# Performance work log

Measured on AMD Instinct MI355X. Metric: run time of the kernel, lower is better.

Reference implementation:

```python
import jax, jax.numpy as jnp
import numpy as np

NUM_CLASSES = 21
OVERLAP_THRESH = 0.5
POS_PRIOR_THRESH = 0.01
NEGPOS_RATIO = 3
ARM_VAR = (0.1, 0.2)
VAR = (0.1, 0.2)
B, P, NOBJ = 64, 16320, 32


def _iou(a, b):
    # a: [N,4] point-form, b: [P,4] point-form -> [N,P]
    lt = jnp.maximum(a[:, None, :2], b[None, :, :2])
    rb = jnp.minimum(a[:, None, 2:], b[None, :, 2:])
    wh = jnp.clip(rb - lt, 0.0)
    inter = wh[..., 0] * wh[..., 1]
    area_a = (a[:, 2] - a[:, 0]) * (a[:, 3] - a[:, 1])
    area_b = (b[:, 2] - b[:, 0]) * (b[:, 3] - b[:, 1])
    return inter / (area_a[:, None] + area_b[None, :] - inter)


def _decode_point(loc, priors, var):
    # loc: [P,4], priors: [P,4] center-form -> [P,4] point-form
    cxcy = priors[:, :2] + loc[:, :2] * var[0] * priors[:, 2:]
    wh = priors[:, 2:] * jnp.exp(loc[:, 2:] * var[1])
    return jnp.concatenate([cxcy - wh / 2, cxcy + wh / 2], axis=-1)


def _encode(matched, priors, var):
    # matched: [P,4] point-form gt, priors: [P,4] center-form -> [P,4]
    g_cxcy = ((matched[:, :2] + matched[:, 2:]) / 2 - priors[:, :2]) / (var[0] * priors[:, 2:])
    g_wh = jnp.log((matched[:, 2:] - matched[:, :2]) / priors[:, 2:]) / var[1]
    return jnp.concatenate([g_cxcy, g_wh], axis=-1)


def _match_one(truths, labels, dec_point, ref_center, reserve):
    # truths:[N,4] labels:[N] dec_point/ref_center:[P,4] reserve:[P] bool
    n_obj = truths.shape[0]
    ov = _iou(truths, dec_point)                       # [N,P]
    ovm = jnp.where(reserve[None, :], ov, -1.0)        # mask out filtered priors
    best_prior_idx = jnp.argmax(ovm, axis=1)           # [N]
    best_truth_overlap = jnp.max(ovm, axis=0)          # [P]
    best_truth_idx = jnp.argmax(ovm, axis=0)           # [P]
    best_truth_overlap = best_truth_overlap.at[best_prior_idx].set(2.0)
    best_truth_idx = best_truth_idx.at[best_prior_idx].set(jnp.arange(n_obj))
    matched = truths[best_truth_idx]                   # [P,4]
    conf = labels[best_truth_idx] + 1                  # [P]
    conf = jnp.where(best_truth_overlap < OVERLAP_THRESH, 0, conf)
    loc = _encode(matched, ref_center, VAR)
    conf = jnp.where(reserve, conf, -1)                # ignored priors
    loc = jnp.where(reserve[:, None], loc, 0.0)
    return loc, conf


def setup_inputs() -> dict:
    key = jax.random.key(0)
    ks = jax.random.split(key, 8)
    arm_loc = 0.1 * jax.random.normal(ks[0], (B, P, 4), dtype=jnp.float32)
    arm_conf = jax.random.normal(ks[1], (B, P, 2), dtype=jnp.float32)
    odm_loc = jax.random.normal(ks[2], (B, P, 4), dtype=jnp.float32)
    odm_conf = jax.random.normal(ks[3], (B, P, NUM_CLASSES), dtype=jnp.float32)
    # center-form anchors: valid cx,cy,w,h
    cxcy = jax.random.uniform(ks[4], (P, 2), minval=0.02, maxval=0.98)
    wh = jax.random.uniform(ks[5], (P, 2), minval=0.05, maxval=0.4)
    priors = jnp.concatenate([cxcy, wh], axis=-1).astype(jnp.float32)
    # valid point-form ground-truth boxes
    tc = jax.random.uniform(ks[6], (B, NOBJ, 2), minval=0.2, maxval=0.8)
    tw = jax.random.uniform(ks[7], (B, NOBJ, 2), minval=0.05, maxval=0.3)
    truths = jnp.concatenate([tc - tw / 2, tc + tw / 2], axis=-1).astype(jnp.float32)
    labels = jax.random.randint(jax.random.fold_in(key, 9), (B, NOBJ), 0, 20)
    return {"arm_loc": arm_loc, "arm_conf": arm_conf, "odm_loc": odm_loc,
            "odm_conf": odm_conf, "priors": priors, "truths": truths,
            "labels": labels}


def reference(arm_loc, arm_conf, odm_loc, odm_conf, priors, truths, labels):
    # ARM branch and targets are constants w.r.t. gradients (torch uses .data)
    arm_loc = jax.lax.stop_gradient(arm_loc)
    arm_conf = jax.lax.stop_gradient(arm_conf)
    truths = jax.lax.stop_gradient(truths)
    priors = jax.lax.stop_gradient(priors)

    arm_pos_prob = jax.nn.softmax(arm_conf, axis=-1)[..., 1]       # [B,P]
    reserve = arm_pos_prob > POS_PRIOR_THRESH                      # [B,P]
    dec_point = jax.vmap(lambda l: _decode_point(l, priors, ARM_VAR))(arm_loc)  # [B,P,4]
    ref_center = jnp.concatenate([(dec_point[..., :2] + dec_point[..., 2:]) / 2,
                                  dec_point[..., 2:] - dec_point[..., :2]], axis=-1)
    loc_t, conf_t = jax.vmap(_match_one)(truths, labels, dec_point, ref_center, reserve)
    loc_t = jax.lax.stop_gradient(loc_t)
    conf_t = jax.lax.stop_gradient(conf_t)

    pos = conf_t > 0                                               # [B,P]
    ignore = conf_t == -1
    conf_t0 = jnp.where(ignore, 0, conf_t)

    # localization: smooth L1 over positives (sum)
    d = jnp.abs(odm_loc - loc_t)
    sl1 = jnp.where(d < 1.0, 0.5 * d * d, d - 0.5)
    loss_l = jnp.sum(sl1 * pos[..., None].astype(sl1.dtype))

    # per-prior CE: logsumexp - target logit
    lse = jax.nn.logsumexp(odm_conf, axis=-1)                      # [B,P]
    tgt = jnp.take_along_axis(odm_conf, conf_t0[..., None], axis=-1)[..., 0]
    ce = lse - tgt                                                 # [B,P]

    # hard-negative mining: rank negatives by CE (double argsort)
    mine = jnp.where(pos | ignore, 0.0, ce)
    order = jnp.argsort(-mine, axis=1)
    rank = jnp.argsort(order, axis=1)
    num_pos = jnp.sum(pos, axis=1, keepdims=True)                  # [B,1]
    num_neg = jnp.minimum(NEGPOS_RATIO * num_pos, P - 1)
    neg = rank < num_neg

    loss_c = jnp.sum(jnp.where(pos | neg, ce, 0.0))
    total_num = jnp.sum(num_pos).astype(jnp.float32)
    return (loss_l / total_num, loss_c / total_num)
```

## Files before the change

### kernel.cpp

```cpp
#include <hip/hip_runtime.h>

#define B 64
#define P 16320
#define NOBJ 32
#define NC 21

__device__ constexpr float LN99 = 4.59511985013459f;

__global__ void k_init(int* num_pos, float* ll_b, float* lc_b) {
    int t = threadIdx.x;
    if (t < B) { num_pos[t] = 0; ll_b[t] = 0.f; lc_b[t] = 0.f; }
}

__global__ __launch_bounds__(1024) void k_p1b(
    const float* __restrict__ arm_loc, const float* __restrict__ arm_conf,
    const float* __restrict__ priors, const float* __restrict__ truths,
    unsigned long long* __restrict__ bp_packed)
{
    int jg = blockIdx.x >> 6;
    int b  = blockIdx.x & 63;
    int tid = threadIdx.x;
    __shared__ unsigned long long s1[8 * 512];
    __shared__ unsigned long long s2[64];

    float4 T[8]; float TA[8];
    #pragma unroll
    for (int jj = 0; jj < 8; jj++) {
        T[jj] = ((const float4*)truths)[b * NOBJ + jg * 8 + jj];
        TA[jj] = (T[jj].z - T[jj].x) * (T[jj].w - T[jj].y);
    }
    unsigned long long key[8];
    #pragma unroll
    for (int jj = 0; jj < 8; jj++) key[jj] = 0x407FFFFFFFFFFFFFULL;

    for (int i = tid; i < P; i += 1024) {
        size_t bpi = (size_t)b * P + i;
        float2 cc = ((const float2*)arm_conf)[bpi];
        bool resv = (cc.x - cc.y) < LN99;
        float4 l = ((const float4*)arm_loc)[bpi];
        float4 pr = ((const float4*)priors)[i];
        float dcx = pr.x + l.x * 0.1f * pr.z;
        float dcy = pr.y + l.y * 0.1f * pr.w;
        float dw = pr.z * __expf(l.z * 0.2f);
        float dh = pr.w * __expf(l.w * 0.2f);
        float x1 = dcx - dw * 0.5f;
        float y1 = dcy - dh * 0.5f;
        float x2 = dcx + dw * 0.5f;
        float y2 = dcy + dh * 0.5f;
        float areaP = (x2 - x1) * (y2 - y1);
        #pragma unroll
        for (int jj = 0; jj < 8; jj++) {
            float iw = fmaxf(fminf(x2, T[jj].z) - fmaxf(x1, T[jj].x), 0.f);
            float ih = fmaxf(fminf(y2, T[jj].w) - fmaxf(y1, T[jj].y), 0.f);
            float inter = iw * ih;
            float iou = inter * __builtin_amdgcn_rcpf(TA[jj] + areaP - inter);
            unsigned long long k =
                ((unsigned long long)(__float_as_uint(iou) | 0x80000000u) << 32)
                | (unsigned)~(unsigned)i;
            if (resv && k > key[jj]) key[jj] = k;
        }
    }

    #pragma unroll
    for (int jj = 0; jj < 8; jj++) {
        unsigned long long o = __shfl_xor(key[jj], 1, 64);
        if (o > key[jj]) key[jj] = o;
    }
    if ((tid & 1) == 0) {
        #pragma unroll
        for (int jj = 0; jj < 8; jj++) s1[jj * 512 + (tid >> 1)] = key[jj];
    }
    __syncthreads();

    unsigned long long m1 = 0;
    {
        int j = tid >> 7, c = tid & 127;
        #pragma unroll
        for (int i = 0; i < 4; i++) {
            unsigned long long v = s1[j * 512 + c * 4 + ((i + c) & 3)];
            if (v > m1) m1 = v;
        }
    }
    __syncthreads();
    s1[tid] = m1;
    __syncthreads();

    if (tid < 64) {
        int j = tid >> 3, c = tid & 7;
        unsigned long long m2 = 0;
        #pragma unroll
        for (int i = 0; i < 16; i++) {
            unsigned long long v = s1[j * 128 + c * 16 + ((i + c) & 15)];
            if (v > m2) m2 = v;
        }
        s2[tid] = m2;
    }
    __syncthreads();

    if (tid < 8) {
        unsigned long long m3 = 0;
        #pragma unroll
        for (int i = 0; i < 8; i++) {
            unsigned long long v = s2[tid * 8 + ((i + tid) & 7)];
            if (v > m3) m3 = v;
        }
        bp_packed[b * NOBJ + jg * 8 + tid] = m3;
    }
}

__global__ __launch_bounds__(256) void k_p2(
    const float* __restrict__ arm_loc, const float* __restrict__ arm_conf,
    const float* __restrict__ odm_loc, const float* __restrict__ odm_conf,
    const float* __restrict__ priors, const float* __restrict__ truths,
    const int* __restrict__ labels,
    const unsigned long long* __restrict__ bp_packed,
    float* __restrict__ mine, int* __restrict__ num_pos,
    float* __restrict__ ll_b, float* __restrict__ lc_b)
{
    int b = blockIdx.y;
    int pbase = blockIdx.x * 256;
    int tid = threadIdx.x;
    int p = pbase + tid;

    __shared__ float soc[256 * NC];
    __shared__ float4 s_tr[NOBJ];
    __shared__ float s_ta[NOBJ];
    __shared__ unsigned s_pi[NOBJ];
    __shared__ int s_lab[NOBJ];

    if (tid < NOBJ) {
        float4 t = ((const float4*)truths)[b * NOBJ + tid];
        s_tr[tid] = t;
        s_ta[tid] = (t.z - t.x) * (t.w - t.y);
        s_pi[tid] = ~(unsigned)(bp_packed[b * NOBJ + tid] & 0xFFFFFFFFULL);
        s_lab[tid] = labels[b * NOBJ + tid];
    }
    {
        int nval = P - pbase; if (nval > 256) nval = 256;
        int tot = nval * NC;
        const float* ocb = odm_conf + ((size_t)b * P + pbase) * NC;
        for (int i = tid; i < tot; i += 256) soc[i] = ocb[i];
    }
    __syncthreads();

    float ll = 0.f, lc = 0.f; int np = 0;
    if (p < P) {
        size_t bpi = (size_t)b * P + p;
        float2 cc = ((const float2*)arm_conf)[bpi];
        bool resv = (cc.x - cc.y) < LN99;

        int bi = 0; bool ge = false;
        float rx1 = 0.f, ry1 = 0.f, rx2 = 0.f, ry2 = 0.f;
        if (resv) {
            float4 l = ((const float4*)arm_loc)[bpi];
            float4 pr = ((const float4*)priors)[p];
            float dcx = pr.x + l.x * 0.1f * pr.z;
            float dcy = pr.y + l.y * 0.1f * pr.w;
            float dw = pr.z * __expf(l.z * 0.2f);
            float dh = pr.w * __expf(l.w * 0.2f);
            rx1 = dcx - dw * 0.5f; ry1 = dcy - dh * 0.5f;
            rx2 = dcx + dw * 0.5f; ry2 = dcy + dh * 0.5f;
            float areaP = (rx2 - rx1) * (ry2 - ry1);
            float bestv = -1.f;
            #pragma unroll
            for (int j = 0; j < NOBJ; j++) {
                float4 t = s_tr[j];
                float iw = fmaxf(fminf(rx2, t.z) - fmaxf(rx1, t.x), 0.f);
                float ih = fmaxf(fminf(ry2, t.w) - fmaxf(ry1, t.y), 0.f);
                float inter = iw * ih;
                float iou = inter * __builtin_amdgcn_rcpf(s_ta[j] + areaP - inter);
                if (iou > bestv) { bestv = iou; bi = j; }
            }
            ge = !(bestv < 0.5f);
        }
        #pragma unroll
        for (int j = 0; j < NOBJ; j++)
            if (s_pi[j] == (unsigned)p) { ge = true; bi = j; }

        int conf = !resv ? -1 : (ge ? s_lab[bi] + 1 : 0);

        const float* row = &soc[tid * NC];
        float m = row[0];
        #pragma unroll
        for (int k = 1; k < NC; k++) m = fmaxf(m, row[k]);
        float s = 0.f;
        #pragma unroll
        for (int k = 0; k < NC; k++) s += __expf(row[k] - m);
        int t0 = conf > 0 ? conf : 0;
        float ce = m + __logf(s) - row[t0];

        bool pos = conf > 0;
        mine[bpi] = (pos || conf == -1) ? 0.f : ce;

        if (pos) {
            np = 1; lc = ce;
            float rcx = (rx1 + rx2) * 0.5f, rcy = (ry1 + ry2) * 0.5f;
            float rw = rx2 - rx1, rh = ry2 - ry1;
            float4 tb = s_tr[bi];
            float g0 = ((tb.x + tb.z) * 0.5f - rcx) * __builtin_amdgcn_rcpf(0.1f * rw);
            float g1 = ((tb.y + tb.w) * 0.5f - rcy) * __builtin_amdgcn_rcpf(0.1f * rh);
            float g2 = __logf((tb.z - tb.x) * __builtin_amdgcn_rcpf(rw)) * 5.0f;
            float g3 = __logf((tb.w - tb.y) * __builtin_amdgcn_rcpf(rh)) * 5.0f;
            float4 ol = ((const float4*)odm_loc)[bpi];
            float gt[4] = {g0, g1, g2, g3};
            float od[4] = {ol.x, ol.y, ol.z, ol.w};
            #pragma unroll
            for (int k = 0; k < 4; k++) {
                float d = fabsf(od[k] - gt[k]);
                ll += (d < 1.f) ? 0.5f * d * d : d - 0.5f;
            }
        }
    }

    #pragma unroll
    for (int off = 32; off; off >>= 1) {
        ll += __shfl_xor(ll, off, 64);
        lc += __shfl_xor(lc, off, 64);
        np += __shfl_xor(np, off, 64);
    }
    __shared__ float sll[4], slc[4];
    __shared__ int snp[4];
    int wid = tid >> 6, lane = tid & 63;
    if (lane == 0) { sll[wid] = ll; slc[wid] = lc; snp[wid] = np; }
    __syncthreads();
    if (tid == 0) {
        float a = 0.f, c = 0.f; int n = 0;
        for (int w = 0; w < 4; w++) { a += sll[w]; c += slc[w]; n += snp[w]; }
        if (a != 0.f) atomicAdd(&ll_b[b], a);
        if (c != 0.f) atomicAdd(&lc_b[b], c);
        if (n) atomicAdd(&num_pos[b], n);
    }
}

__global__ __launch_bounds__(256) void k_select(
    const float* __restrict__ mine, const int* __restrict__ num_pos,
    float* __restrict__ lc_b)
{
    int b = blockIdx.x;
    int tid = threadIdx.x;
    int K0 = num_pos[b] * 3;
    if (K0 > P - 1) K0 = P - 1;
    if (K0 <= 0) return;
    const float* row = mine + (size_t)b * P;

    __shared__ unsigned hist[256];
    __shared__ unsigned s_beta, s_K;

    unsigned K = (unsigned)K0;
    unsigned prefix = 0, maskDone = 0;

    for (int pass = 0; pass < 4; pass++) {
        int shift = 24 - pass * 8;
        hist[tid] = 0;
        __syncthreads();
        for (int i = tid; i < P; i += 256) {
            unsigned bits = __float_as_uint(row[i]);
            if ((bits & maskDone) == prefix) atomicAdd(&hist[(bits >> shift) & 255u], 1u);
        }
        __syncthreads();
        if (tid < 64) {
            unsigned u0 = hist[tid * 4 + 0], u1 = hist[tid * 4 + 1];
            unsigned u2 = hist[tid * 4 + 2], u3 = hist[tid * 4 + 3];
            unsigned sum4 = u0 + u1 + u2 + u3;
            unsigned x = sum4;
            #pragma unroll
            for (int off = 1; off < 64; off <<= 1) {
                unsigned y = __shfl_down(x, off, 64);
                if (tid + off < 64) x += y;
            }
            unsigned sf0 = x, sf1 = x - u0, sf2 = x - u0 - u1, sf3 = x - u0 - u1 - u2;
            unsigned sf4 = x - sum4;
            if (sf0 >= K && sf1 < K) { s_beta = tid * 4 + 0; s_K = K - sf1; }
            if (sf1 >= K && sf2 < K) { s_beta = tid * 4 + 1; s_K = K - sf2; }
            if (sf2 >= K && sf3 < K) { s_beta = tid * 4 + 2; s_K = K - sf3; }
            if (sf3 >= K && sf4 < K) { s_beta = tid * 4 + 3; s_K = K - sf4; }
        }
        __syncthreads();
        prefix |= (s_beta << shift);
        maskDone |= (0xFFu << shift);
        K = s_K;
        __syncthreads();
    }

    unsigned tBits = prefix;
    float t = __uint_as_float(tBits);

    unsigned mcnt = 0; float ssum = 0.f;
    for (int i = tid; i < P; i += 256) {
        float v = row[i];
        if (__float_as_uint(v) > tBits) { mcnt++; ssum += v; }
    }
    #pragma unroll
    for (int off = 32; off; off >>= 1) {
        mcnt += __shfl_xor(mcnt, off, 64);
        ssum += __shfl_xor(ssum, off, 64);
    }
    __shared__ float sS[4];
    __shared__ unsigned sM[4];
    int wid = tid >> 6, lane = tid & 63;
    if (lane == 0) { sS[wid] = ssum; sM[wid] = mcnt; }
    __syncthreads();
    if (tid == 0) {
        float S = 0.f; unsigned M = 0;
        for (int w = 0; w < 4; w++) { S += sS[w]; M += sM[w]; }
        atomicAdd(&lc_b[b], S + (float)(K0 - (int)M) * t);
    }
}

__global__ void k_final(const int* __restrict__ num_pos, const float* __restrict__ ll_b,
                        const float* __restrict__ lc_b, float* __restrict__ out) {
    int t = threadIdx.x;
    int np = num_pos[t];
    float ll = ll_b[t];
    float lc = lc_b[t];
    #pragma unroll
    for (int off = 32; off; off >>= 1) {
        np += __shfl_xor(np, off, 64);
        ll += __shfl_xor(ll, off, 64);
        lc += __shfl_xor(lc, off, 64);
    }
    if (t == 0) {
        float tn = (float)np;
        out[0] = ll / tn;
        out[1] = lc / tn;
    }
}

extern "C" void kernel_launch(void* const* d_in, const int* in_sizes, int n_in,
                              void* d_out, int out_size, void* d_ws, size_t ws_size,
                              hipStream_t stream) {
    const float* arm_loc  = (const float*)d_in[0];
    const float* arm_conf = (const float*)d_in[1];
    const float* odm_loc  = (const float*)d_in[2];
    const float* odm_conf = (const float*)d_in[3];
    const float* priors   = (const float*)d_in[4];
    const float* truths   = (const float*)d_in[5];
    const int*   labels   = (const int*)d_in[6];
    float* out = (float*)d_out;

    char* ws = (char*)d_ws;
    const size_t BPTOT = (size_t)B * P;
    float* mine = (float*)ws;
    unsigned long long* bp_packed = (unsigned long long*)(ws + 4ull * BPTOT);
    int*   num_pos = (int*)(ws + 4ull * BPTOT + 8ull * B * NOBJ);
    float* ll_b    = (float*)(ws + 4ull * BPTOT + 8ull * B * NOBJ + 4ull * B);
    float* lc_b    = (float*)(ws + 4ull * BPTOT + 8ull * B * NOBJ + 8ull * B);

    k_init<<<1, 64, 0, stream>>>(num_pos, ll_b, lc_b);
    k_p1b<<<256, 1024, 0, stream>>>(arm_loc, arm_conf, priors, truths, bp_packed);
    k_p2<<<dim3(64, B), 256, 0, stream>>>(arm_loc, arm_conf, odm_loc, odm_conf,
                                          priors, truths, labels, bp_packed,
                                          mine, num_pos, ll_b, lc_b);
    k_select<<<B, 256, 0, stream>>>(mine, num_pos, lc_b);
    k_final<<<1, 64, 0, stream>>>(num_pos, ll_b, lc_b, out);
}
```

Before: 281.9 us.

## Compute full prior-truth IoU once in matching pass and stage select row in LDS

The first kernel now splits each image's priors into four chunks and computes IoU against all 32 truths in one pass. It produces both the per-truth best prior (as per-chunk partial maxima) and a packed per-prior best-truth/threshold/reserve word. The second kernel no longer recomputes the 32-way IoU or reads arm_conf, and instead reads the packed word and merges the partial maxima into an LDS override table. It also copies odm_conf with float4 loads. The top-k select kernel uses 1024 threads, caches the whole row in LDS, and uses per-wave histograms to cut atomic contention, at the cost of extra workspace traffic and more LDS.

```diff
diff --git a/kernel.cpp b/kernel.cpp
--- a/kernel.cpp
+++ b/kernel.cpp
@@ -4,116 +4,129 @@
 #define P 16320
 #define NOBJ 32
 #define NC 21
+#define CHUNK 4080
 
 __device__ constexpr float LN99 = 4.59511985013459f;
+#define SENT 0x407FFFFFFFFFFFFFULL
 
 __global__ void k_init(int* num_pos, float* ll_b, float* lc_b) {
     int t = threadIdx.x;
     if (t < B) { num_pos[t] = 0; ll_b[t] = 0.f; lc_b[t] = 0.f; }
 }
 
-__global__ __launch_bounds__(1024) void k_p1b(
+__global__ __launch_bounds__(1024) void k_p1(
     const float* __restrict__ arm_loc, const float* __restrict__ arm_conf,
     const float* __restrict__ priors, const float* __restrict__ truths,
-    unsigned long long* __restrict__ bp_packed)
+    int* __restrict__ bt_pack, unsigned long long* __restrict__ bp_part)
 {
-    int jg = blockIdx.x >> 6;
-    int b  = blockIdx.x & 63;
+    int b = blockIdx.x >> 2, c = blockIdx.x & 3;
     int tid = threadIdx.x;
-    __shared__ unsigned long long s1[8 * 512];
-    __shared__ unsigned long long s2[64];
-
-    float4 T[8]; float TA[8];
-    #pragma unroll
-    for (int jj = 0; jj < 8; jj++) {
-        T[jj] = ((const float4*)truths)[b * NOBJ + jg * 8 + jj];
-        TA[jj] = (T[jj].z - T[jj].x) * (T[jj].w - T[jj].y);
-    }
-    unsigned long long key[8];
-    #pragma unroll
-    for (int jj = 0; jj < 8; jj++) key[jj] = 0x407FFFFFFFFFFFFFULL;
-
-    for (int i = tid; i < P; i += 1024) {
-        size_t bpi = (size_t)b * P + i;
-        float2 cc = ((const float2*)arm_conf)[bpi];
-        bool resv = (cc.x - cc.y) < LN99;
-        float4 l = ((const float4*)arm_loc)[bpi];
-        float4 pr = ((const float4*)priors)[i];
-        float dcx = pr.x + l.x * 0.1f * pr.z;
-        float dcy = pr.y + l.y * 0.1f * pr.w;
-        float dw = pr.z * __expf(l.z * 0.2f);
-        float dh = pr.w * __expf(l.w * 0.2f);
-        float x1 = dcx - dw * 0.5f;
-        float y1 = dcy - dh * 0.5f;
-        float x2 = dcx + dw * 0.5f;
-        float y2 = dcy + dh * 0.5f;
-        float areaP = (x2 - x1) * (y2 - y1);
-        #pragma unroll
-        for (int jj = 0; jj < 8; jj++) {
-            float iw = fmaxf(fminf(x2, T[jj].z) - fmaxf(x1, T[jj].x), 0.f);
-            float ih = fmaxf(fminf(y2, T[jj].w) - fmaxf(y1, T[jj].y), 0.f);
+    int base = c * CHUNK;
+
+    __shared__ float4 s_tr[NOBJ];
+    __shared__ float s_ta[NOBJ];
+    __shared__ unsigned long long s1[NOBJ * 256];
+    __shared__ unsigned long long s2[1024];
+
+    if (tid < NOBJ) {
+        float4 t = ((const float4*)truths)[b * NOBJ + tid];
+        s_tr[tid] = t;
+        s_ta[tid] = (t.z - t.x) * (t.w - t.y);
+    }
+    __syncthreads();
+
+    float x1[4], y1[4], x2[4], y2[4], ap[4];
+    bool rs[4], av[4];
+    #pragma unroll
+    for (int g = 0; g < 4; g++) {
+        int off = g * 1024 + tid;
+        av[g] = off < CHUNK;
+        rs[g] = false;
+        x1[g] = y1[g] = x2[g] = y2[g] = ap[g] = 0.f;
+        if (av[g]) {
+            int p = base + off;
+            size_t bpi = (size_t)b * P + p;
+            float2 cc = ((const float2*)arm_conf)[bpi];
+            rs[g] = (cc.x - cc.y) < LN99;
+            float4 l = ((const float4*)arm_loc)[bpi];
+            float4 pr = ((const float4*)priors)[p];
+            float dcx = pr.x + l.x * 0.1f * pr.z;
+            float dcy = pr.y + l.y * 0.1f * pr.w;
+            float dw = pr.z * __expf(l.z * 0.2f);
+            float dh = pr.w * __expf(l.w * 0.2f);
+            x1[g] = dcx - dw * 0.5f; y1[g] = dcy - dh * 0.5f;
+            x2[g] = dcx + dw * 0.5f; y2[g] = dcy + dh * 0.5f;
+            ap[g] = (x2[g] - x1[g]) * (y2[g] - y1[g]);
+        }
+    }
+
+    float bv[4] = {-1.f, -1.f, -1.f, -1.f};
+    int bj[4] = {0, 0, 0, 0};
+
+    #pragma unroll
+    for (int j = 0; j < NOBJ; j++) {
+        float4 t = s_tr[j];
+        float ta = s_ta[j];
+        float jv = -1.f; int jg = 0;
+        #pragma unroll
+        for (int g = 0; g < 4; g++) {
+            float iw = fmaxf(fminf(x2[g], t.z) - fmaxf(x1[g], t.x), 0.f);
+            float ih = fmaxf(fminf(y2[g], t.w) - fmaxf(y1[g], t.y), 0.f);
             float inter = iw * ih;
-            float iou = inter * __builtin_amdgcn_rcpf(TA[jj] + areaP - inter);
-            unsigned long long k =
-                ((unsigned long long)(__float_as_uint(iou) | 0x80000000u) << 32)
-                | (unsigned)~(unsigned)i;
-            if (resv && k > key[jj]) key[jj] = k;
-        }
-    }
-
-    #pragma unroll
-    for (int jj = 0; jj < 8; jj++) {
-        unsigned long long o = __shfl_xor(key[jj], 1, 64);
-        if (o > key[jj]) key[jj] = o;
-    }
-    if ((tid & 1) == 0) {
-        #pragma unroll
-        for (int jj = 0; jj < 8; jj++) s1[jj * 512 + (tid >> 1)] = key[jj];
-    }
-    __syncthreads();
-
-    unsigned long long m1 = 0;
+            float iou = inter * __builtin_amdgcn_rcpf(ta + ap[g] - inter);
+            float iou_r = av[g] ? iou : -1.f;
+            if (iou_r > bv[g]) { bv[g] = iou_r; bj[g] = j; }
+            float iou_m = rs[g] ? iou_r : -1.f;
+            if (iou_m > jv) { jv = iou_m; jg = g; }
+        }
+        unsigned long long pk = 0ULL;
+        if (jv >= 0.f) {
+            unsigned p = (unsigned)(base + jg * 1024 + tid);
+            pk = ((unsigned long long)(__float_as_uint(jv) | 0x80000000u) << 32)
+               | (unsigned)~p;
+        }
+        { unsigned long long o = __shfl_xor(pk, 1, 64); if (o > pk) pk = o; }
+        { unsigned long long o = __shfl_xor(pk, 2, 64); if (o > pk) pk = o; }
+        if ((tid & 3) == 0) s1[j * 256 + (tid >> 2)] = pk;
+    }
+
+    #pragma unroll
+    for (int g = 0; g < 4; g++) {
+        if (av[g]) {
+            int p = base + g * 1024 + tid;
+            int bt = rs[g] ? ((bj[g] << 2) | ((bv[g] >= 0.5f) ? 2 : 0) | 1) : 0;
+            bt_pack[(size_t)b * P + p] = bt;
+        }
+    }
+    __syncthreads();
+
     {
-        int j = tid >> 7, c = tid & 127;
-        #pragma unroll
-        for (int i = 0; i < 4; i++) {
-            unsigned long long v = s1[j * 512 + c * 4 + ((i + c) & 3)];
-            if (v > m1) m1 = v;
-        }
-    }
-    __syncthreads();
-    s1[tid] = m1;
-    __syncthreads();
-
-    if (tid < 64) {
-        int j = tid >> 3, c = tid & 7;
-        unsigned long long m2 = 0;
-        #pragma unroll
-        for (int i = 0; i < 16; i++) {
-            unsigned long long v = s1[j * 128 + c * 16 + ((i + c) & 15)];
-            if (v > m2) m2 = v;
-        }
-        s2[tid] = m2;
-    }
-    __syncthreads();
-
-    if (tid < 8) {
-        unsigned long long m3 = 0;
-        #pragma unroll
-        for (int i = 0; i < 8; i++) {
-            unsigned long long v = s2[tid * 8 + ((i + tid) & 7)];
-            if (v > m3) m3 = v;
-        }
-        bp_packed[b * NOBJ + jg * 8 + tid] = m3;
+        int j = tid >> 5, r = tid & 31;
+        unsigned long long m = 0;
+        #pragma unroll
+        for (int q = 0; q < 8; q++) {
+            unsigned long long v = s1[j * 256 + q * 32 + r];
+            if (v > m) m = v;
+        }
+        s2[tid] = m;
+    }
+    __syncthreads();
+    if (tid < NOBJ) {
+        unsigned long long m = 0;
+        #pragma unroll
+        for (int i = 0; i < 32; i++) {
+            unsigned long long v = s2[tid * 32 + ((i + tid) & 31)];
+            if (v > m) m = v;
+        }
+        bp_part[blockIdx.x * NOBJ + tid] = m;
     }
 }
 
 __global__ __launch_bounds__(256) void k_p2(
-    const float* __restrict__ arm_loc, const float* __restrict__ arm_conf,
-    const float* __restrict__ odm_loc, const float* __restrict__ odm_conf,
-    const float* __restrict__ priors, const float* __restrict__ truths,
-    const int* __restrict__ labels,
-    const unsigned long long* __restrict__ bp_packed,
+    const float* __restrict__ arm_loc, const float* __restrict__ odm_loc,
+    const float* __restrict__ odm_conf, const float* __restrict__ priors,
+    const float* __restrict__ truths, const int* __restrict__ labels,
+    const int* __restrict__ bt_pack, const unsigned long long* __restrict__ bp_part,
     float* __restrict__ mine, int* __restrict__ num_pos,
     float* __restrict__ ll_b, float* __restrict__ lc_b)
 {
@@ -124,76 +137,70 @@
 
     __shared__ float soc[256 * NC];
     __shared__ float4 s_tr[NOBJ];
-    __shared__ float s_ta[NOBJ];
-    __shared__ unsigned s_pi[NOBJ];
     __shared__ int s_lab[NOBJ];
-
+    __shared__ int s_ov[256];
+
+    s_ov[tid] = -1;
     if (tid < NOBJ) {
         float4 t = ((const float4*)truths)[b * NOBJ + tid];
         s_tr[tid] = t;
-        s_ta[tid] = (t.z - t.x) * (t.w - t.y);
-        s_pi[tid] = ~(unsigned)(bp_packed[b * NOBJ + tid] & 0xFFFFFFFFULL);
         s_lab[tid] = labels[b * NOBJ + tid];
     }
     {
         int nval = P - pbase; if (nval > 256) nval = 256;
-        int tot = nval * NC;
-        const float* ocb = odm_conf + ((size_t)b * P + pbase) * NC;
-        for (int i = tid; i < tot; i += 256) soc[i] = ocb[i];
+        int tot4 = (nval * NC) >> 2;
+        const float4* src = (const float4*)(odm_conf + ((size_t)b * P + pbase) * NC);
+        float4* dst = (float4*)soc;
+        for (int i = tid; i < tot4; i += 256) dst[i] = src[i];
+    }
+    __syncthreads();
+
+    if (tid < NOBJ) {
+        unsigned long long m = SENT;
+        #pragma unroll
+        for (int c = 0; c < 4; c++) {
+            unsigned long long v = bp_part[(b * 4 + c) * NOBJ + tid];
+            if (v > m) m = v;
+        }
+        int pi = (int)~(unsigned)(m & 0xFFFFFFFFULL);
+        if (pi >= pbase && pi < pbase + 256) atomicMax(&s_ov[pi - pbase], tid);
     }
     __syncthreads();
 
     float ll = 0.f, lc = 0.f; int np = 0;
     if (p < P) {
         size_t bpi = (size_t)b * P + p;
-        float2 cc = ((const float2*)arm_conf)[bpi];
-        bool resv = (cc.x - cc.y) < LN99;
-
-        int bi = 0; bool ge = false;
-        float rx1 = 0.f, ry1 = 0.f, rx2 = 0.f, ry2 = 0.f;
-        if (resv) {
+        int bt = bt_pack[bpi];
+        bool resv = bt & 1;
+        int ge = (bt >> 1) & 1;
+        int bi = bt >> 2;
+        int ov = s_ov[tid];
+        if (ov >= 0) { ge = 1; bi = ov; }
+
+        int conf = !resv ? -1 : (ge ? s_lab[bi] + 1 : 0);
+
+        const float* row = &soc[tid * NC];
+        float mx = row[0];
+        #pragma unroll
+        for (int k = 1; k < NC; k++) mx = fmaxf(mx, row[k]);
+        float s = 0.f;
+        #pragma unroll
+        for (int k = 0; k < NC; k++) s += __expf(row[k] - mx);
+        int t0 = conf > 0 ? conf : 0;
+        float ce = mx + __logf(s) - row[t0];
+
+        mine[bpi] = (conf == 0) ? ce : 0.f;
+
+        if (conf > 0) {
+            np = 1; lc = ce;
             float4 l = ((const float4*)arm_loc)[bpi];
             float4 pr = ((const float4*)priors)[p];
             float dcx = pr.x + l.x * 0.1f * pr.z;
             float dcy = pr.y + l.y * 0.1f * pr.w;
             float dw = pr.z * __expf(l.z * 0.2f);
             float dh = pr.w * __expf(l.w * 0.2f);
-            rx1 = dcx - dw * 0.5f; ry1 = dcy - dh * 0.5f;
-            rx2 = dcx + dw * 0.5f; ry2 = dcy + dh * 0.5f;
-            float areaP = (rx2 - rx1) * (ry2 - ry1);
-            float bestv = -1.f;
-            #pragma unroll
-            for (int j = 0; j < NOBJ; j++) {
-                float4 t = s_tr[j];
-                float iw = fmaxf(fminf(rx2, t.z) - fmaxf(rx1, t.x), 0.f);
-                float ih = fmaxf(fminf(ry2, t.w) - fmaxf(ry1, t.y), 0.f);
-                float inter = iw * ih;
-                float iou = inter * __builtin_amdgcn_rcpf(s_ta[j] + areaP - inter);
-                if (iou > bestv) { bestv = iou; bi = j; }
-            }
-            ge = !(bestv < 0.5f);
-        }
-        #pragma unroll
-        for (int j = 0; j < NOBJ; j++)
-            if (s_pi[j] == (unsigned)p) { ge = true; bi = j; }
-
-        int conf = !resv ? -1 : (ge ? s_lab[bi] + 1 : 0);
-
-        const float* row = &soc[tid * NC];
-        float m = row[0];
-        #pragma unroll
-        for (int k = 1; k < NC; k++) m = fmaxf(m, row[k]);
-        float s = 0.f;
-        #pragma unroll
-        for (int k = 0; k < NC; k++) s += __expf(row[k] - m);
-        int t0 = conf > 0 ? conf : 0;
-        float ce = m + __logf(s) - row[t0];
-
-        bool pos = conf > 0;
-        mine[bpi] = (pos || conf == -1) ? 0.f : ce;
-
-        if (pos) {
-            np = 1; lc = ce;
+            float rx1 = dcx - dw * 0.5f, ry1 = dcy - dh * 0.5f;
+            float rx2 = dcx + dw * 0.5f, ry2 = dcy + dh * 0.5f;
             float rcx = (rx1 + rx2) * 0.5f, rcy = (ry1 + ry2) * 0.5f;
             float rw = rx2 - rx1, rh = ry2 - ry1;
             float4 tb = s_tr[bi];
@@ -224,43 +231,61 @@
     if (lane == 0) { sll[wid] = ll; slc[wid] = lc; snp[wid] = np; }
     __syncthreads();
     if (tid == 0) {
-        float a = 0.f, c = 0.f; int n = 0;
-        for (int w = 0; w < 4; w++) { a += sll[w]; c += slc[w]; n += snp[w]; }
+        float a = 0.f, cq = 0.f; int n = 0;
+        for (int w = 0; w < 4; w++) { a += sll[w]; cq += slc[w]; n += snp[w]; }
         if (a != 0.f) atomicAdd(&ll_b[b], a);
-        if (c != 0.f) atomicAdd(&lc_b[b], c);
+        if (cq != 0.f) atomicAdd(&lc_b[b], cq);
         if (n) atomicAdd(&num_pos[b], n);
     }
 }
 
-__global__ __launch_bounds__(256) void k_select(
+__global__ __launch_bounds__(1024) void k_select(
     const float* __restrict__ mine, const int* __restrict__ num_pos,
     float* __restrict__ lc_b)
 {
-    int b = blockIdx.x;
-    int tid = threadIdx.x;
+    int b = blockIdx.x, tid = threadIdx.x;
     int K0 = num_pos[b] * 3;
     if (K0 > P - 1) K0 = P - 1;
     if (K0 <= 0) return;
-    const float* row = mine + (size_t)b * P;
-
-    __shared__ unsigned hist[256];
+
+    __shared__ float4 s_row4[P / 4];
+    __shared__ unsigned hist[16 * 257];
+    __shared__ unsigned s_merged[256];
     __shared__ unsigned s_beta, s_K;
-
-    unsigned K = (unsigned)K0;
-    unsigned prefix = 0, maskDone = 0;
+    __shared__ float sS[16];
+    __shared__ unsigned sM[16];
+
+    const float4* src = (const float4*)(mine + (size_t)b * P);
+    for (int i = tid; i < P / 4; i += 1024) s_row4[i] = src[i];
+
+    unsigned K = (unsigned)K0, prefix = 0, maskDone = 0;
+    int wid = tid >> 6;
 
     for (int pass = 0; pass < 4; pass++) {
         int shift = 24 - pass * 8;
-        hist[tid] = 0;
-        __syncthreads();
-        for (int i = tid; i < P; i += 256) {
-            unsigned bits = __float_as_uint(row[i]);
-            if ((bits & maskDone) == prefix) atomicAdd(&hist[(bits >> shift) & 255u], 1u);
+        for (int i = tid; i < 16 * 257; i += 1024) hist[i] = 0;
+        __syncthreads();
+        for (int i = tid; i < P / 4; i += 1024) {
+            float4 v = s_row4[i];
+            float vv[4] = {v.x, v.y, v.z, v.w};
+            #pragma unroll
+            for (int e = 0; e < 4; e++) {
+                unsigned bits = __float_as_uint(vv[e]);
+                if ((bits & maskDone) == prefix)
+                    atomicAdd(&hist[wid * 257 + ((bits >> shift) & 255u)], 1u);
+            }
+        }
+        __syncthreads();
+        if (tid < 256) {
+            unsigned t = 0;
+            #pragma unroll
+            for (int w = 0; w < 16; w++) t += hist[w * 257 + tid];
+            s_merged[tid] = t;
         }
         __syncthreads();
         if (tid < 64) {
-            unsigned u0 = hist[tid * 4 + 0], u1 = hist[tid * 4 + 1];
-            unsigned u2 = hist[tid * 4 + 2], u3 = hist[tid * 4 + 3];
+            unsigned u0 = s_merged[tid * 4 + 0], u1 = s_merged[tid * 4 + 1];
+            unsigned u2 = s_merged[tid * 4 + 2], u3 = s_merged[tid * 4 + 3];
             unsigned sum4 = u0 + u1 + u2 + u3;
             unsigned x = sum4;
             #pragma unroll
@@ -286,23 +311,25 @@
     float t = __uint_as_float(tBits);
 
     unsigned mcnt = 0; float ssum = 0.f;
-    for (int i = tid; i < P; i += 256) {
-        float v = row[i];
-        if (__float_as_uint(v) > tBits) { mcnt++; ssum += v; }
+    for (int i = tid; i < P / 4; i += 1024) {
+        float4 v = s_row4[i];
+        float vv[4] = {v.x, v.y, v.z, v.w};
+        #pragma unroll
+        for (int e = 0; e < 4; e++) {
+            if (__float_as_uint(vv[e]) > tBits) { mcnt++; ssum += vv[e]; }
+        }
     }
     #pragma unroll
     for (int off = 32; off; off >>= 1) {
         mcnt += __shfl_xor(mcnt, off, 64);
         ssum += __shfl_xor(ssum, off, 64);
     }
-    __shared__ float sS[4];
-    __shared__ unsigned sM[4];
-    int wid = tid >> 6, lane = tid & 63;
+    int lane = tid & 63;
     if (lane == 0) { sS[wid] = ssum; sM[wid] = mcnt; }
     __syncthreads();
     if (tid == 0) {
         float S = 0.f; unsigned M = 0;
-        for (int w = 0; w < 4; w++) { S += sS[w]; M += sM[w]; }
+        for (int w = 0; w < 16; w++) { S += sS[w]; M += sM[w]; }
         atomicAdd(&lc_b[b], S + (float)(K0 - (int)M) * t);
     }
 }
@@ -340,17 +367,19 @@
 
     char* ws = (char*)d_ws;
     const size_t BPTOT = (size_t)B * P;
-    float* mine = (float*)ws;
-    unsigned long long* bp_packed = (unsigned long long*)(ws + 4ull * BPTOT);
-    int*   num_pos = (int*)(ws + 4ull * BPTOT + 8ull * B * NOBJ);
-    float* ll_b    = (float*)(ws + 4ull * BPTOT + 8ull * B * NOBJ + 4ull * B);
-    float* lc_b    = (float*)(ws + 4ull * BPTOT + 8ull * B * NOBJ + 8ull * B);
+    float* mine    = (float*)ws;
+    int*   bt_pack = (int*)(ws + 4ull * BPTOT);
+    unsigned long long* bp_part = (unsigned long long*)(ws + 8ull * BPTOT);
+    int*   num_pos = (int*)(ws + 8ull * BPTOT + 65536ull);
+    float* ll_b    = (float*)(ws + 8ull * BPTOT + 65536ull + 256ull);
+    float* lc_b    = (float*)(ws + 8ull * BPTOT + 65536ull + 512ull);
 
     k_init<<<1, 64, 0, stream>>>(num_pos, ll_b, lc_b);
-    k_p1b<<<256, 1024, 0, stream>>>(arm_loc, arm_conf, priors, truths, bp_packed);
-    k_p2<<<dim3(64, B), 256, 0, stream>>>(arm_loc, arm_conf, odm_loc, odm_conf,
-                                          priors, truths, labels, bp_packed,
+    k_p1<<<256, 1024, 0, stream>>>(arm_loc, arm_conf, priors, truths,
+                                   bt_pack, bp_part);
+    k_p2<<<dim3(64, B), 256, 0, stream>>>(arm_loc, odm_loc, odm_conf, priors,
+                                          truths, labels, bt_pack, bp_part,
                                           mine, num_pos, ll_b, lc_b);
-    k_select<<<B, 256, 0, stream>>>(mine, num_pos, lc_b);
+    k_select<<<B, 1024, 0, stream>>>(mine, num_pos, lc_b);
     k_final<<<1, 64, 0, stream>>>(num_pos, ll_b, lc_b, out);
 }
```

Result: faster. 248.9 us (-11.7%).
